# Performance work log

Measured on AMD Instinct MI355X. Metric: run time of the kernel, lower is better.

The kernel has to match this reference:

```python
import jax, jax.numpy as jnp
import numpy as np

FIXED_POINT = 4
LOGMAX = 7
MAX_INT8 = 127
B, H = 16384, 2048


def _clipped_add(*ts):
    r = ts[0].astype(jnp.int32)
    for t in ts[1:]:
        r = r + t.astype(jnp.int32)
    return jnp.clip(r, -MAX_INT8, MAX_INT8).astype(jnp.int8)


def _int_matmul(x, w):
    # x: (..., in) int8, w: (out, in) int8 -> (..., out) int8
    r = jnp.matmul(x.astype(jnp.int32), w.T.astype(jnp.int32))
    scale = (2 ** FIXED_POINT) * int(np.sqrt(w.shape[-1]))  # 16 * 45 = 720 for H=2048
    r = r // scale  # floor division, matches torch // on ints
    return jnp.clip(r, -MAX_INT8, MAX_INT8).astype(jnp.int8)


def setup_inputs() -> dict:
    key = jax.random.key(0)
    k_x, k_s, k_wf, k_uf, k_wh, k_uh = jax.random.split(key, 6)

    def init_w(k):
        w = jax.random.normal(k, (H, H), dtype=jnp.float32) * (2 ** FIXED_POINT)
        return jnp.clip(jnp.round(w), -MAX_INT8, MAX_INT8).astype(jnp.int8)

    x = jax.random.randint(k_x, (B, H), -MAX_INT8, MAX_INT8 + 1, dtype=jnp.int32).astype(jnp.int8)
    state = jax.random.randint(k_s, (B, H), -MAX_INT8, MAX_INT8 + 1, dtype=jnp.int32).astype(jnp.int8)
    return {
        "x": x,
        "state": state,
        "W_f": init_w(k_wf),
        "U_f": init_w(k_uf),
        "b_f": jnp.zeros((H,), dtype=jnp.int8),
        "W_h": init_w(k_wh),
        "U_h": init_w(k_uh),
        "b_h": jnp.zeros((H,), dtype=jnp.int8),
    }


def reference(x, state, W_f, U_f, b_f, W_h, U_h, b_h):
    f_t = _clipped_add(_int_matmul(x, W_f), _int_matmul(state, U_f), b_f)
    f_gate = f_t.astype(jnp.int32) + MAX_INT8  # in [0, 254]
    # note: torch `a >> LOGMAX + 1` parses as a >> (LOGMAX + 1) == >> 8 (arithmetic shift)
    gated_past = (f_gate * state.astype(jnp.int32)) >> (LOGMAX + 1)
    gated_past = jnp.clip(gated_past, -MAX_INT8, MAX_INT8).astype(jnp.int8)
    h_tilde = _clipped_add(_int_matmul(x, W_h), _int_matmul(gated_past, U_h), b_h)
    diff = h_tilde.astype(jnp.int32) - state.astype(jnp.int32)
    new_state = state.astype(jnp.int32) + ((f_gate * diff) >> (LOGMAX + 1))
    new_state = jnp.clip(new_state, -MAX_INT8, MAX_INT8).astype(jnp.int8)
    return (new_state, new_state)
```

## Files before the change

kernel.cpp:

```cpp
#include <hip/hip_runtime.h>
#include <stdint.h>

#define HH 2048
#define BB 16384
#define NK (HH / 64)

typedef int v4i __attribute__((ext_vector_type(4)));

__device__ __forceinline__ int clip127(int v){
  v = v > 127 ? 127 : v;
  return v < -127 ? -127 : v;
}
__device__ __forceinline__ int fdiv720(int r){
  int q = r / 720;
  return q - ((r - q * 720) < 0 ? 1 : 0);
}

__global__ void pack_i32_to_i8(const int* __restrict__ src, int8_t* __restrict__ dst, int n16){
  int stride = gridDim.x * blockDim.x;
  for (int i = blockIdx.x * blockDim.x + threadIdx.x; i < n16; i += stride){
    const int4* s = (const int4*)src + (size_t)i * 4;
    int4 a = s[0], b = s[1], c = s[2], d = s[3];
    int4 o;
    o.x = (a.x & 255) | ((a.y & 255) << 8) | ((a.z & 255) << 16) | (a.w << 24);
    o.y = (b.x & 255) | ((b.y & 255) << 8) | ((b.z & 255) << 16) | (b.w << 24);
    o.z = (c.x & 255) | ((c.y & 255) << 8) | ((c.z & 255) << 16) | (c.w << 24);
    o.w = (d.x & 255) | ((d.y & 255) << 8) | ((d.z & 255) << 16) | (d.w << 24);
    ((int4*)dst)[i] = o;
  }
}

__global__ void dup_out(const int* __restrict__ src, int* __restrict__ dst, int n4){
  int stride = gridDim.x * blockDim.x;
  for (int i = blockIdx.x * blockDim.x + threadIdx.x; i < n4; i += stride)
    ((int4*)dst)[i] = ((const int4*)src)[i];
}

template<int PHASE>
__global__ __launch_bounds__(256, 2)
void gemm_dual(const int8_t* __restrict__ A1, const int8_t* __restrict__ A2,
               const int8_t* __restrict__ B1, const int8_t* __restrict__ B2,
               const int* __restrict__ bias,
               const int8_t* __restrict__ state8,
               int* fbuf, int8_t* __restrict__ g8out, int* __restrict__ out2)
{
  __shared__ __align__(16) int8_t lds[2 * 32768];
  const int tid  = threadIdx.x;
  const int lane = tid & 63;
  const int wave = tid >> 6;
  const int wrow = wave >> 1, wcol = wave & 1;

  const int bid = blockIdx.x;
  const int wg  = (bid & 7) * 256 + (bid >> 3);
  const int rowbase = (wg >> 4) * 128;
  const int colbase = (wg & 15) * 128;

  v4i accA[4][4], accB[4][4];
  const v4i vzero = {0, 0, 0, 0};
#pragma unroll
  for (int m = 0; m < 4; m++)
#pragma unroll
    for (int n = 0; n < 4; n++){ accA[m][n] = vzero; accB[m][n] = vzero; }

  const int srow   = tid >> 2;
  const int schunk = tid & 3;
  const int chunk  = lane >> 4;
  const int rl     = lane & 15;

  auto STAGE = [&](int buf, int kk){
    const int k0 = kk * 64;
    const int bb = buf * 32768;
#pragma unroll
    for (int p = 0; p < 2; p++){
      const int row = p * 64 + srow;
      const int swc = schunk ^ ((row >> 1) & 3);
      const size_t aoff = (size_t)(rowbase + row) * HH + k0 + swc * 16;
      const size_t boff = (size_t)(colbase + row) * HH + k0 + swc * 16;
      const int ldst = bb + p * 4096 + tid * 16;
      __builtin_amdgcn_global_load_lds((const __attribute__((address_space(1))) void*)(A1 + aoff),
                                       (__attribute__((address_space(3))) void*)(lds + ldst), 16, 0, 0);
      __builtin_amdgcn_global_load_lds((const __attribute__((address_space(1))) void*)(A2 + aoff),
                                       (__attribute__((address_space(3))) void*)(lds + 8192 + ldst), 16, 0, 0);
      __builtin_amdgcn_global_load_lds((const __attribute__((address_space(1))) void*)(B1 + boff),
                                       (__attribute__((address_space(3))) void*)(lds + 16384 + ldst), 16, 0, 0);
      __builtin_amdgcn_global_load_lds((const __attribute__((address_space(1))) void*)(B2 + boff),
                                       (__attribute__((address_space(3))) void*)(lds + 24576 + ldst), 16, 0, 0);
    }
  };

  int cur = 0;
  STAGE(0, 0);
  __syncthreads();

  for (int kk = 0; kk < NK; ++kk){
    if (kk + 1 < NK) STAGE(cur ^ 1, kk + 1);
    const int cb = cur * 32768;
    {
      v4i af[4], bf[4];
#pragma unroll
      for (int m = 0; m < 4; m++){
        const int row = wrow * 64 + m * 16 + rl;
        af[m] = *(const v4i*)(lds + cb + row * 64 + ((chunk ^ ((row >> 1) & 3)) << 4));
      }
#pragma unroll
      for (int n = 0; n < 4; n++){
        const int row = wcol * 64 + n * 16 + rl;
        bf[n] = *(const v4i*)(lds + cb + 16384 + row * 64 + ((chunk ^ ((row >> 1) & 3)) << 4));
      }
#pragma unroll
      for (int m = 0; m < 4; m++)
#pragma unroll
        for (int n = 0; n < 4; n++)
          accA[m][n] = __builtin_amdgcn_mfma_i32_16x16x64_i8(af[m], bf[n], accA[m][n], 0, 0, 0);
    }
    {
      v4i af[4], bf[4];
#pragma unroll
      for (int m = 0; m < 4; m++){
        const int row = wrow * 64 + m * 16 + rl;
        af[m] = *(const v4i*)(lds + cb + 8192 + row * 64 + ((chunk ^ ((row >> 1) & 3)) << 4));
      }
#pragma unroll
      for (int n = 0; n < 4; n++){
        const int row = wcol * 64 + n * 16 + rl;
        bf[n] = *(const v4i*)(lds + cb + 24576 + row * 64 + ((chunk ^ ((row >> 1) & 3)) << 4));
      }
#pragma unroll
      for (int m = 0; m < 4; m++)
#pragma unroll
        for (int n = 0; n < 4; n++)
          accB[m][n] = __builtin_amdgcn_mfma_i32_16x16x64_i8(af[m], bf[n], accB[m][n], 0, 0, 0);
    }
    __syncthreads();
    cur ^= 1;
  }

  const int q = lane >> 4;
#pragma unroll
  for (int m = 0; m < 4; m++){
#pragma unroll
    for (int n = 0; n < 4; n++){
      const int gcol = colbase + wcol * 64 + n * 16 + rl;
      const int bval = bias[gcol];
#pragma unroll
      for (int r = 0; r < 4; r++){
        const int grow = rowbase + wrow * 64 + m * 16 + q * 4 + r;
        const size_t idx = (size_t)grow * HH + gcol;
        const int v1 = clip127(fdiv720(accA[m][n][r]));
        const int v2 = clip127(fdiv720(accB[m][n][r]));
        const int t  = clip127(v1 + v2 + bval);
        const int st = state8[idx];
        if (PHASE == 1){
          const int fg = t + 127;
          fbuf[idx]  = fg;
          g8out[idx] = (int8_t)clip127((fg * st) >> 8);
        } else {
          const int fg = fbuf[idx];
          const int ns = clip127(st + ((fg * (t - st)) >> 8));
          fbuf[idx] = ns;
          if (out2) out2[idx] = ns;
        }
      }
    }
  }
}

extern "C" void kernel_launch(void* const* d_in, const int* in_sizes, int n_in,
                              void* d_out, int out_size, void* d_ws, size_t ws_size,
                              hipStream_t stream){
  const int* x  = (const int*)d_in[0];
  const int* st = (const int*)d_in[1];
  const int* Wf = (const int*)d_in[2];
  const int* Uf = (const int*)d_in[3];
  const int* bf = (const int*)d_in[4];
  const int* Wh = (const int*)d_in[5];
  const int* Uh = (const int*)d_in[6];
  const int* bh = (const int*)d_in[7];

  const size_t NBH = (size_t)BB * HH;
  const size_t NW  = (size_t)HH * HH;
  const size_t need = 3 * NBH + 4 * NW;

  int*    out1   = (int*)d_out;
  const bool wsp = (ws_size >= need);
  int8_t* base   = wsp ? (int8_t*)d_ws : (int8_t*)d_out + NBH * 4;
  int8_t* x8  = base;
  int8_t* s8  = x8 + NBH;
  int8_t* g8  = s8 + NBH;
  int8_t* wf8 = g8 + NBH;
  int8_t* uf8 = wf8 + NW;
  int8_t* wh8 = uf8 + NW;
  int8_t* uh8 = wh8 + NW;

  pack_i32_to_i8<<<2048, 256, 0, stream>>>(x,  x8,  (int)(NBH / 16));
  pack_i32_to_i8<<<2048, 256, 0, stream>>>(st, s8,  (int)(NBH / 16));
  pack_i32_to_i8<<<1024, 256, 0, stream>>>(Wf, wf8, (int)(NW / 16));
  pack_i32_to_i8<<<1024, 256, 0, stream>>>(Uf, uf8, (int)(NW / 16));
  pack_i32_to_i8<<<1024, 256, 0, stream>>>(Wh, wh8, (int)(NW / 16));
  pack_i32_to_i8<<<1024, 256, 0, stream>>>(Uh, uh8, (int)(NW / 16));

  gemm_dual<1><<<2048, 256, 0, stream>>>(x8, s8, wf8, uf8, bf, s8, out1, g8, nullptr);
  gemm_dual<2><<<2048, 256, 0, stream>>>(x8, g8, wh8, uh8, bh, s8, out1, nullptr,
                                         wsp ? out1 + NBH : nullptr);

  if (!wsp)
    dup_out<<<2048, 256, 0, stream>>>(out1, out1 + NBH, (int)(NBH / 4));
}
```

Baseline: 621.8 us.

## Use 8-wave blocks with single-buffered LDS to raise occupancy

The dual GEMM kernel moves from 256 to 512 threads per block, with 8 waves in a 2x4 layout that each own a 64x32 output sub-tile, which halves accumulator registers per wave. The LDS double buffer is dropped for a single 32 KB buffer, and the staging now loads and syncs before computing each k-step. The intent is higher occupancy (launch bounds 512,4) so other waves hide global-to-LDS latency. The cost is that loads no longer overlap compute within a block, and there is an extra barrier per iteration.

```diff
diff --git a/kernel.cpp b/kernel.cpp
--- a/kernel.cpp
+++ b/kernel.cpp
@@ -37,110 +37,99 @@
 }
 
 template<int PHASE>
-__global__ __launch_bounds__(256, 2)
+__global__ __launch_bounds__(512, 4)
 void gemm_dual(const int8_t* __restrict__ A1, const int8_t* __restrict__ A2,
                const int8_t* __restrict__ B1, const int8_t* __restrict__ B2,
                const int* __restrict__ bias,
                const int8_t* __restrict__ state8,
                int* fbuf, int8_t* __restrict__ g8out, int* __restrict__ out2)
 {
-  __shared__ __align__(16) int8_t lds[2 * 32768];
+  __shared__ __align__(16) int8_t lds[32768];
   const int tid  = threadIdx.x;
   const int lane = tid & 63;
   const int wave = tid >> 6;
-  const int wrow = wave >> 1, wcol = wave & 1;
+  const int wrow = wave >> 2;
+  const int wcol = wave & 3;
 
   const int bid = blockIdx.x;
   const int wg  = (bid & 7) * 256 + (bid >> 3);
   const int rowbase = (wg >> 4) * 128;
   const int colbase = (wg & 15) * 128;
 
-  v4i accA[4][4], accB[4][4];
+  v4i accA[4][2], accB[4][2];
   const v4i vzero = {0, 0, 0, 0};
 #pragma unroll
   for (int m = 0; m < 4; m++)
 #pragma unroll
-    for (int n = 0; n < 4; n++){ accA[m][n] = vzero; accB[m][n] = vzero; }
+    for (int n = 0; n < 2; n++){ accA[m][n] = vzero; accB[m][n] = vzero; }
 
   const int srow   = tid >> 2;
   const int schunk = tid & 3;
   const int chunk  = lane >> 4;
   const int rl     = lane & 15;
 
-  auto STAGE = [&](int buf, int kk){
-    const int k0 = kk * 64;
-    const int bb = buf * 32768;
-#pragma unroll
-    for (int p = 0; p < 2; p++){
-      const int row = p * 64 + srow;
-      const int swc = schunk ^ ((row >> 1) & 3);
-      const size_t aoff = (size_t)(rowbase + row) * HH + k0 + swc * 16;
-      const size_t boff = (size_t)(colbase + row) * HH + k0 + swc * 16;
-      const int ldst = bb + p * 4096 + tid * 16;
-      __builtin_amdgcn_global_load_lds((const __attribute__((address_space(1))) void*)(A1 + aoff),
-                                       (__attribute__((address_space(3))) void*)(lds + ldst), 16, 0, 0);
-      __builtin_amdgcn_global_load_lds((const __attribute__((address_space(1))) void*)(A2 + aoff),
-                                       (__attribute__((address_space(3))) void*)(lds + 8192 + ldst), 16, 0, 0);
-      __builtin_amdgcn_global_load_lds((const __attribute__((address_space(1))) void*)(B1 + boff),
-                                       (__attribute__((address_space(3))) void*)(lds + 16384 + ldst), 16, 0, 0);
-      __builtin_amdgcn_global_load_lds((const __attribute__((address_space(1))) void*)(B2 + boff),
-                                       (__attribute__((address_space(3))) void*)(lds + 24576 + ldst), 16, 0, 0);
-    }
-  };
-
-  int cur = 0;
-  STAGE(0, 0);
-  __syncthreads();
+  const int  swc   = schunk ^ ((srow >> 1) & 3);
+  const size_t aoff0 = (size_t)(rowbase + srow) * HH + swc * 16;
+  const size_t boff0 = (size_t)(colbase + srow) * HH + swc * 16;
+  const int  ldst  = tid * 16;
 
   for (int kk = 0; kk < NK; ++kk){
-    if (kk + 1 < NK) STAGE(cur ^ 1, kk + 1);
-    const int cb = cur * 32768;
+    const int k0 = kk * 64;
+    __builtin_amdgcn_global_load_lds((const __attribute__((address_space(1))) void*)(A1 + aoff0 + k0),
+                                     (__attribute__((address_space(3))) void*)(lds + ldst), 16, 0, 0);
+    __builtin_amdgcn_global_load_lds((const __attribute__((address_space(1))) void*)(A2 + aoff0 + k0),
+                                     (__attribute__((address_space(3))) void*)(lds + 8192 + ldst), 16, 0, 0);
+    __builtin_amdgcn_global_load_lds((const __attribute__((address_space(1))) void*)(B1 + boff0 + k0),
+                                     (__attribute__((address_space(3))) void*)(lds + 16384 + ldst), 16, 0, 0);
+    __builtin_amdgcn_global_load_lds((const __attribute__((address_space(1))) void*)(B2 + boff0 + k0),
+                                     (__attribute__((address_space(3))) void*)(lds + 24576 + ldst), 16, 0, 0);
+    __syncthreads();
+
     {
-      v4i af[4], bf[4];
+      v4i af[4], bf[2];
 #pragma unroll
       for (int m = 0; m < 4; m++){
         const int row = wrow * 64 + m * 16 + rl;
-        af[m] = *(const v4i*)(lds + cb + row * 64 + ((chunk ^ ((row >> 1) & 3)) << 4));
+        af[m] = *(const v4i*)(lds + row * 64 + ((chunk ^ ((row >> 1) & 3)) << 4));
       }
 #pragma unroll
-      for (int n = 0; n < 4; n++){
-        const int row = wcol * 64 + n * 16 + rl;
-        bf[n] = *(const v4i*)(lds + cb + 16384 + row * 64 + ((chunk ^ ((row >> 1) & 3)) << 4));
+      for (int n = 0; n < 2; n++){
+        const int row = wcol * 32 + n * 16 + rl;
+        bf[n] = *(const v4i*)(lds + 16384 + row * 64 + ((chunk ^ ((row >> 1) & 3)) << 4));
       }
 #pragma unroll
       for (int m = 0; m < 4; m++)
 #pragma unroll
-        for (int n = 0; n < 4; n++)
+        for (int n = 0; n < 2; n++)
           accA[m][n] = __builtin_amdgcn_mfma_i32_16x16x64_i8(af[m], bf[n], accA[m][n], 0, 0, 0);
     }
     {
-      v4i af[4], bf[4];
+      v4i af[4], bf[2];
 #pragma unroll
       for (int m = 0; m < 4; m++){
         const int row = wrow * 64 + m * 16 + rl;
-        af[m] = *(const v4i*)(lds + cb + 8192 + row * 64 + ((chunk ^ ((row >> 1) & 3)) << 4));
+        af[m] = *(const v4i*)(lds + 8192 + row * 64 + ((chunk ^ ((row >> 1) & 3)) << 4));
       }
 #pragma unroll
-      for (int n = 0; n < 4; n++){
-        const int row = wcol * 64 + n * 16 + rl;
-        bf[n] = *(const v4i*)(lds + cb + 24576 + row * 64 + ((chunk ^ ((row >> 1) & 3)) << 4));
+      for (int n = 0; n < 2; n++){
+        const int row = wcol * 32 + n * 16 + rl;
+        bf[n] = *(const v4i*)(lds + 24576 + row * 64 + ((chunk ^ ((row >> 1) & 3)) << 4));
       }
 #pragma unroll
       for (int m = 0; m < 4; m++)
 #pragma unroll
-        for (int n = 0; n < 4; n++)
+        for (int n = 0; n < 2; n++)
           accB[m][n] = __builtin_amdgcn_mfma_i32_16x16x64_i8(af[m], bf[n], accB[m][n], 0, 0, 0);
     }
     __syncthreads();
-    cur ^= 1;
   }
 
   const int q = lane >> 4;
 #pragma unroll
   for (int m = 0; m < 4; m++){
 #pragma unroll
-    for (int n = 0; n < 4; n++){
-      const int gcol = colbase + wcol * 64 + n * 16 + rl;
+    for (int n = 0; n < 2; n++){
+      const int gcol = colbase + wcol * 32 + n * 16 + rl;
       const int bval = bias[gcol];
 #pragma unroll
       for (int r = 0; r < 4; r++){
@@ -199,8 +188,8 @@
   pack_i32_to_i8<<<1024, 256, 0, stream>>>(Wh, wh8, (int)(NW / 16));
   pack_i32_to_i8<<<1024, 256, 0, stream>>>(Uh, uh8, (int)(NW / 16));
 
-  gemm_dual<1><<<2048, 256, 0, stream>>>(x8, s8, wf8, uf8, bf, s8, out1, g8, nullptr);
-  gemm_dual<2><<<2048, 256, 0, stream>>>(x8, g8, wh8, uh8, bh, s8, out1, nullptr,
+  gemm_dual<1><<<2048, 512, 0, stream>>>(x8, s8, wf8, uf8, bf, s8, out1, g8, nullptr);
+  gemm_dual<2><<<2048, 512, 0, stream>>>(x8, g8, wh8, uh8, bh, s8, out1, nullptr,
                                          wsp ? out1 + NBH : nullptr);
 
   if (!wsp)
```

New measurement: 590.9 us. -5.0%, faster.
